# Optimization experiments

Hardware: AMD Instinct MI355X
Metric: run time of the kernel (lower is better)

Reference implementation:

```python
import jax, jax.numpy as jnp
import numpy as np

N_NODES = 100000
N_EDGES = 800000
D_IN, D_HID, D_OUT = 128, 128, 128


def sage_conv(x, edge_index, Wl, bl, Wr):
    # PyG SAGEConv with mean aggregation:
    #   out = lin_l(mean_{j in N(i)} x_j) + lin_r(x_i)
    # x: [N, Din], edge_index: [2, E] (src=row0 -> dst=row1)
    src, dst = edge_index[0], edge_index[1]
    n = x.shape[0]
    msg_sum = jax.ops.segment_sum(x[src], dst, num_segments=n)        # [N, Din]
    deg = jax.ops.segment_sum(jnp.ones((src.shape[0],), x.dtype), dst,
                              num_segments=n)                          # [N]
    agg = msg_sum / jnp.maximum(deg, 1.0)[:, None]
    return agg @ Wl + bl + x @ Wr


def setup_inputs() -> dict:
    key = jax.random.key(0)
    ks = jax.random.split(key, 8)
    s = 1.0 / np.sqrt(D_IN)
    return {
        "x": jax.random.normal(ks[0], (3, N_NODES, D_IN), jnp.float32),
        "edge_index": jax.random.randint(ks[1], (3, 2, N_EDGES), 0, N_NODES,
                                         dtype=jnp.int64),
        "Wl1": jax.random.normal(ks[2], (3, D_IN, D_HID), jnp.float32) * s,
        "bl1": jax.random.normal(ks[3], (3, D_HID), jnp.float32) * s,
        "Wr1": jax.random.normal(ks[4], (3, D_IN, D_HID), jnp.float32) * s,
        "Wl2": jax.random.normal(ks[5], (3, D_HID, D_OUT), jnp.float32) * s,
        "bl2": jax.random.normal(ks[6], (3, D_OUT), jnp.float32) * s,
        "Wr2": jax.random.normal(ks[7], (3, D_HID, D_OUT), jnp.float32) * s,
    }


def reference(x, edge_index, Wl1, bl1, Wr1, Wl2, bl2, Wr2):
    # vmap over the 3 graphs (user-item, social, knowledge)
    conv = jax.vmap(sage_conv)
    h = jax.nn.relu(conv(x, edge_index, Wl1, bl1, Wr1))   # [3, N, hid]
    out = conv(h, edge_index, Wl2, bl2, Wr2)              # [3, N, out]
    # x = ui_x + (s_x + k_x) / 2
    return out[0] + (out[1] + out[2]) / 2
```

## Files before the change

kernel.cpp:

```cpp
#include <hip/hip_runtime.h>

#define N_NODES 100000
#define N_EDGES 800000
#define D 128
#define NBUCK 98
#define CAP 10240
#define QBLK 18750
#define S2B 196
#define QSC 2048.0f
#define IQSC (1.0f / 2048.0f)

typedef __attribute__((ext_vector_type(8))) short short8;
typedef __attribute__((ext_vector_type(4))) float float4_t;
typedef unsigned short ushort_t;

#define MFMA __builtin_amdgcn_mfma_f32_16x16x32_bf16

__device__ __forceinline__ float b2fu(unsigned short u) {
    unsigned int v = ((unsigned int)u) << 16;
    return __builtin_bit_cast(float, v);
}
__device__ __forceinline__ unsigned short f2b(float f) {
    unsigned int u = __builtin_bit_cast(unsigned int, f);
    u = u + 0x7fffu + ((u >> 16) & 1u);
    return (unsigned short)(u >> 16);
}
__device__ __forceinline__ void splitf(float x, unsigned short& h, unsigned short& l) {
    h = f2b(x);
    l = f2b(x - b2fu(h));
}
__device__ __forceinline__ void cvtsplit8(short8 qv, short8& hh, short8& ll) {
#pragma unroll
    for (int j = 0; j < 8; j++) {
        float f = (float)qv[j] * IQSC;
        unsigned short h, l;
        splitf(f, h, l);
        hh[j] = (short)h;
        ll[j] = (short)l;
    }
}

__global__ void setup_kernel(const unsigned int* __restrict__ w, int* __restrict__ flag,
                             int* __restrict__ bucketCount) {
    int t = threadIdx.x;
    if (t == 0) flag[0] = 0;
    for (int i = t; i < 3 * NBUCK; i += 256) bucketCount[i] = 0;
    __syncthreads();
    int any = 0;
    for (int i = t; i < 4096; i += 256)
        if (w[2 * i + 1] != 0) any = 1;
    if (any) atomicOr(flag, 1);
}

__device__ __forceinline__ int ld_idx(const int* w, int f, long j) {
    return f ? w[j] : w[2 * j];
}

__global__ __launch_bounds__(256) void s2q_kernel(const float* __restrict__ X,
                                                  short* __restrict__ XS,
                                                  const int* __restrict__ ei,
                                                  const int* __restrict__ flag,
                                                  int* __restrict__ bucketCount,
                                                  unsigned int* __restrict__ tmp) {
    __shared__ int hist[NBUCK];
    __shared__ int cnt[NBUCK];
    int bxa = blockIdx.x;
    if (bxa < QBLK) {
        size_t i = (size_t)bxa * 256 + threadIdx.x;
        float4 u0 = *(const float4*)(X + i * 8);
        float4 u1 = *(const float4*)(X + i * 8 + 4);
        float vv[8] = {u0.x, u0.y, u0.z, u0.w, u1.x, u1.y, u1.z, u1.w};
        short8 qv;
#pragma unroll
        for (int j = 0; j < 8; j++) {
            int q = __float2int_rn(vv[j] * QSC);
            q = max(-32767, min(32767, q));
            qv[j] = (short)q;
        }
        *(short8*)(XS + i * 8) = qv;
        return;
    }
    int b = bxa - QBLK;
    int g = b / S2B, bx = b % S2B;
    int t = threadIdx.x;
    const int f = flag[0];
    const long j0 = (long)g * 2 * N_EDGES;
    if (t < NBUCK) hist[t] = 0;
    __syncthreads();
#pragma unroll
    for (int it = 0; it < 16; it++) {
        int e = bx * 4096 + it * 256 + t;
        if (e < N_EDGES) {
            int dst = ld_idx(ei, f, j0 + N_EDGES + e);
            atomicAdd(&hist[dst >> 10], 1);
        }
    }
    __syncthreads();
    if (t < NBUCK) cnt[t] = atomicAdd(&bucketCount[g * NBUCK + t], hist[t]);
    __syncthreads();
#pragma unroll
    for (int it = 0; it < 16; it++) {
        int e = bx * 4096 + it * 256 + t;
        if (e < N_EDGES) {
            int src = ld_idx(ei, f, j0 + e);
            int dst = ld_idx(ei, f, j0 + N_EDGES + e);
            int bk = dst >> 10;
            int r = atomicAdd(&cnt[bk], 1);
            if (r < CAP)
                tmp[(size_t)(g * NBUCK + bk) * CAP + r] =
                    (unsigned)src | ((unsigned)(dst & 1023) << 17);
        }
    }
}

__global__ __launch_bounds__(1024) void s3_csr_kernel(const unsigned int* __restrict__ tmp,
                                                      const int* __restrict__ bucketCount,
                                                      int* __restrict__ rowptr,
                                                      int* __restrict__ col) {
    __shared__ int sm[1024];
    __shared__ int pr[1024];
    __shared__ int sbase;
    int b = blockIdx.x, g = blockIdx.y, t = threadIdx.x;
    pr[t] = 0;
    if (t < 128) sm[t] = (t < NBUCK) ? bucketCount[g * NBUCK + t] : 0;
    __syncthreads();
    if (t == 0) {
        int a = 0;
        for (int i = 0; i < b; i++) a += sm[i];
        sbase = a;
    }
    __syncthreads();
    int count = bucketCount[g * NBUCK + b];
    if (count > CAP) count = CAP;
    const unsigned int* recs = tmp + (size_t)(g * NBUCK + b) * CAP;
    for (int i = t; i < count; i += 1024) atomicAdd(&pr[recs[i] >> 17], 1);
    __syncthreads();
    int h = pr[t];
    sm[t] = h;
    __syncthreads();
    for (int off = 1; off < 1024; off <<= 1) {
        int u = (t >= off) ? sm[t - off] : 0;
        __syncthreads();
        sm[t] += u;
        __syncthreads();
    }
    int excl = sm[t] - h;
    int base = sbase;
    int node = b * 1024 + t;
    if (node < N_NODES) rowptr[g * (N_NODES + 1) + node] = base + excl;
    if (b == NBUCK - 1 && t == 0) rowptr[g * (N_NODES + 1) + N_NODES] = N_EDGES;
    __syncthreads();
    pr[t] = base + excl;
    __syncthreads();
    for (int i = t; i < count; i += 1024) {
        unsigned int rec = recs[i];
        int pos = atomicAdd(&pr[rec >> 17], 1);
        col[(size_t)g * N_EDGES + pos] = (int)(rec & 0x1FFFFu);
    }
}

__global__ void packB_kernel(const float* __restrict__ Wl1, const float* __restrict__ Wr1,
                             const float* __restrict__ Wl2, const float* __restrict__ Wr2,
                             ushort_t* __restrict__ Bph, ushort_t* __restrict__ Bpl) {
    int lane = threadIdx.x;
    int tb = blockIdx.x;
    int pidx = blockIdx.y;
    int g = pidx >> 1, layer = pidx & 1;
    const float* Wl = (layer ? Wl2 : Wl1) + (size_t)g * D * D;
    const float* Wr = (layer ? Wr2 : Wr1) + (size_t)g * D * D;
    float scale = (layer && g > 0) ? 0.5f : 1.0f;
    int ks = tb >> 3, nt = tb & 7;
    int n = nt * 16 + (lane & 15);
    int kb = ks * 32 + ((lane >> 4) * 8);
    short8 vh, vl;
#pragma unroll
    for (int j = 0; j < 8; j++) {
        int k = kb + j;
        float wv = ((k < D) ? Wl[k * D + n] : Wr[(k - D) * D + n]) * scale;
        unsigned short h, l;
        splitf(wv, h, l);
        vh[j] = (short)h;
        vl[j] = (short)l;
    }
    size_t o = ((size_t)pidx * 4096 + tb * 64 + lane) * 8;
    *(short8*)(Bph + o) = vh;
    *(short8*)(Bpl + o) = vl;
}

__global__ __launch_bounds__(256) void agg_kernel(const int* __restrict__ rowptr,
                                                  const int* __restrict__ col,
                                                  const short* __restrict__ XS,
                                                  short* __restrict__ AS) {
    int g = blockIdx.y;
    int wid = (int)((blockIdx.x * 256 + threadIdx.x) >> 6);
    if (wid >= N_NODES) return;
    int lane = threadIdx.x & 63;
    int qw = lane >> 4, l4 = lane & 15;
    const int* rp = rowptr + (size_t)g * (N_NODES + 1);
    const int* cle = col + (size_t)g * N_EDGES;
    const short* Xg = XS + (size_t)g * N_NODES * 128;
    int s = rp[wid], e = rp[wid + 1];
    int a0 = 0, a1 = 0, a2 = 0, a3 = 0, a4 = 0, a5 = 0, a6 = 0, a7 = 0;
    for (int i = s + qw; i < e; i += 16) {
        bool p1 = (i + 4) < e, p2 = (i + 8) < e, p3 = (i + 12) < e;
        int c0 = cle[i];
        int c1 = p1 ? cle[i + 4] : c0;
        int c2 = p2 ? cle[i + 8] : c0;
        int c3 = p3 ? cle[i + 12] : c0;
        int4 z = {0, 0, 0, 0};
        int4 v0 = *(const int4*)(Xg + (size_t)c0 * 128 + l4 * 8);
        int4 v1 = p1 ? *(const int4*)(Xg + (size_t)c1 * 128 + l4 * 8) : z;
        int4 v2 = p2 ? *(const int4*)(Xg + (size_t)c2 * 128 + l4 * 8) : z;
        int4 v3 = p3 ? *(const int4*)(Xg + (size_t)c3 * 128 + l4 * 8) : z;
        a0 += (short)v0.x + (short)v1.x + (short)v2.x + (short)v3.x;
        a1 += (v0.x >> 16) + (v1.x >> 16) + (v2.x >> 16) + (v3.x >> 16);
        a2 += (short)v0.y + (short)v1.y + (short)v2.y + (short)v3.y;
        a3 += (v0.y >> 16) + (v1.y >> 16) + (v2.y >> 16) + (v3.y >> 16);
        a4 += (short)v0.z + (short)v1.z + (short)v2.z + (short)v3.z;
        a5 += (v0.z >> 16) + (v1.z >> 16) + (v2.z >> 16) + (v3.z >> 16);
        a6 += (short)v0.w + (short)v1.w + (short)v2.w + (short)v3.w;
        a7 += (v0.w >> 16) + (v1.w >> 16) + (v2.w >> 16) + (v3.w >> 16);
    }
    a0 += __shfl_xor(a0, 16); a1 += __shfl_xor(a1, 16);
    a2 += __shfl_xor(a2, 16); a3 += __shfl_xor(a3, 16);
    a4 += __shfl_xor(a4, 16); a5 += __shfl_xor(a5, 16);
    a6 += __shfl_xor(a6, 16); a7 += __shfl_xor(a7, 16);
    a0 += __shfl_xor(a0, 32); a1 += __shfl_xor(a1, 32);
    a2 += __shfl_xor(a2, 32); a3 += __shfl_xor(a3, 32);
    a4 += __shfl_xor(a4, 32); a5 += __shfl_xor(a5, 32);
    a6 += __shfl_xor(a6, 32); a7 += __shfl_xor(a7, 32);
    if (lane < 16) {
        float invd = (e > s) ? 1.f / (float)(e - s) : 0.f;
        int m0 = __float2int_rn((float)a0 * invd);
        int m1 = __float2int_rn((float)a1 * invd);
        int m2 = __float2int_rn((float)a2 * invd);
        int m3 = __float2int_rn((float)a3 * invd);
        int m4 = __float2int_rn((float)a4 * invd);
        int m5 = __float2int_rn((float)a5 * invd);
        int m6 = __float2int_rn((float)a6 * invd);
        int m7 = __float2int_rn((float)a7 * invd);
        uint4 st;
        st.x = (m0 & 0xffff) | (m1 << 16);
        st.y = (m2 & 0xffff) | (m3 << 16);
        st.z = (m4 & 0xffff) | (m5 << 16);
        st.w = (m6 & 0xffff) | (m7 << 16);
        *(uint4*)(AS + ((size_t)g * N_NODES + wid) * 128 + l4 * 8) = st;
    }
}

__device__ __forceinline__ void gemm_pass(const short* __restrict__ Agg,
                                          const short* __restrict__ Self,
                                          const short8* __restrict__ GH,
                                          const short8* __restrict__ GL,
                                          short8* smH, short8* smL,
                                          int n0, int t, int lane, bool valid,
                                          float4_t acc[2][8]) {
    int r0 = lane & 15, koff = (lane >> 4) * 8;
#pragma unroll
    for (int ks = 0; ks < 8; ks++) {
        __syncthreads();
        smH[t] = GH[ks * 512 + t];
        smH[t + 256] = GH[ks * 512 + t + 256];
        smL[t] = GL[ks * 512 + t];
        smL[t + 256] = GL[ks * 512 + t + 256];
        __syncthreads();
        if (valid) {
            int kk = (ks & 3) * 32 + koff;
            const short* P = (ks < 4) ? Agg : Self;
            short8 q0 = *(const short8*)(P + (size_t)(n0 + r0) * 128 + kk);
            short8 q1 = *(const short8*)(P + (size_t)(n0 + r0 + 16) * 128 + kk);
            short8 a0h, a0l, a1h, a1l;
            cvtsplit8(q0, a0h, a0l);
            cvtsplit8(q1, a1h, a1l);
#pragma unroll
            for (int nt = 0; nt < 8; nt++) {
                short8 wh = smH[nt * 64 + lane];
                short8 wl = smL[nt * 64 + lane];
                acc[0][nt] = MFMA(a0h, wh, acc[0][nt], 0, 0, 0);
                acc[0][nt] = MFMA(a0l, wh, acc[0][nt], 0, 0, 0);
                acc[0][nt] = MFMA(a0h, wl, acc[0][nt], 0, 0, 0);
                acc[1][nt] = MFMA(a1h, wh, acc[1][nt], 0, 0, 0);
                acc[1][nt] = MFMA(a1l, wh, acc[1][nt], 0, 0, 0);
                acc[1][nt] = MFMA(a1h, wl, acc[1][nt], 0, 0, 0);
            }
        }
    }
}

__global__ __launch_bounds__(256) void gemm1_kernel(const short* __restrict__ AS,
                                                    const short* __restrict__ XS,
                                                    const ushort_t* __restrict__ Bph,
                                                    const ushort_t* __restrict__ Bpl,
                                                    const float* __restrict__ bl1,
                                                    short* __restrict__ HS) {
    __shared__ short8 smH[512];
    __shared__ short8 smL[512];
    int g = blockIdx.y;
    int t = threadIdx.x, w = t >> 6, lane = t & 63;
    int n0 = blockIdx.x * 128 + w * 32;
    bool valid = (n0 < N_NODES);

    float4_t acc[2][8];
#pragma unroll
    for (int m = 0; m < 2; m++)
#pragma unroll
        for (int nt = 0; nt < 8; nt++) acc[m][nt] = (float4_t)(0.f);

    gemm_pass(AS + (size_t)g * N_NODES * 128, XS + (size_t)g * N_NODES * 128,
              (const short8*)Bph + (size_t)(g * 2) * 4096,
              (const short8*)Bpl + (size_t)(g * 2) * 4096,
              smH, smL, n0, t, lane, valid, acc);

    if (!valid) return;
    int qq = lane >> 4, c = lane & 15;
    short* Hg = HS + (size_t)g * N_NODES * 128;
#pragma unroll
    for (int m = 0; m < 2; m++)
#pragma unroll
        for (int nt = 0; nt < 8; nt++) {
            int clm = nt * 16 + c;
            float bv = bl1[g * D + clm];
#pragma unroll
            for (int r = 0; r < 4; r++) {
                int row = n0 + m * 16 + qq * 4 + r;
                float v = fmaxf(acc[m][nt][r] + bv, 0.f);
                int qv = __float2int_rn(v * QSC);
                qv = min(qv, 32767);
                Hg[(size_t)row * 128 + clm] = (short)qv;
            }
        }
}

__global__ __launch_bounds__(256) void gemm2_kernel(const short* __restrict__ AS,
                                                    const short* __restrict__ HS,
                                                    const ushort_t* __restrict__ Bph,
                                                    const ushort_t* __restrict__ Bpl,
                                                    const float* __restrict__ bl2,
                                                    float* __restrict__ out) {
    __shared__ short8 smH[512];
    __shared__ short8 smL[512];
    int t = threadIdx.x, w = t >> 6, lane = t & 63;
    int n0 = blockIdx.x * 128 + w * 32;
    bool valid = (n0 < N_NODES);

    float4_t acc[2][8];
#pragma unroll
    for (int m = 0; m < 2; m++)
#pragma unroll
        for (int nt = 0; nt < 8; nt++) acc[m][nt] = (float4_t)(0.f);

#pragma unroll 1
    for (int g = 0; g < 3; g++) {
        gemm_pass(AS + (size_t)g * N_NODES * 128, HS + (size_t)g * N_NODES * 128,
                  (const short8*)Bph + (size_t)(g * 2 + 1) * 4096,
                  (const short8*)Bpl + (size_t)(g * 2 + 1) * 4096,
                  smH, smL, n0, t, lane, valid, acc);
    }

    if (!valid) return;
    int qq = lane >> 4, c = lane & 15;
#pragma unroll
    for (int m = 0; m < 2; m++)
#pragma unroll
        for (int nt = 0; nt < 8; nt++) {
            int clm = nt * 16 + c;
            float bv = bl2[clm] + 0.5f * (bl2[D + clm] + bl2[2 * D + clm]);
#pragma unroll
            for (int r = 0; r < 4; r++) {
                int row = n0 + m * 16 + qq * 4 + r;
                out[(size_t)row * D + clm] = acc[m][nt][r] + bv;
            }
        }
}

extern "C" void kernel_launch(void* const* d_in, const int* in_sizes, int n_in,
                              void* d_out, int out_size, void* d_ws, size_t ws_size,
                              hipStream_t stream) {
    const float* x   = (const float*)d_in[0];
    const int* ei    = (const int*)d_in[1];
    const float* Wl1 = (const float*)d_in[2];
    const float* bl1 = (const float*)d_in[3];
    const float* Wr1 = (const float*)d_in[4];
    const float* Wl2 = (const float*)d_in[5];
    const float* bl2 = (const float*)d_in[6];
    const float* Wr2 = (const float*)d_in[7];
    float* out = (float*)d_out;

    char* p = (char*)d_ws;
    auto alloc = [&](size_t bytes) -> char* {
        char* r = p;
        p += (bytes + 255) & ~(size_t)255;
        return r;
    };
    int* flag        = (int*)alloc(256);
    int* bucketCount = (int*)alloc((size_t)3 * NBUCK * 4);
    int* rowptr      = (int*)alloc((size_t)3 * (N_NODES + 1) * 4);
    int* col         = (int*)alloc((size_t)3 * N_EDGES * 4);
    ushort_t* Bph    = (ushort_t*)alloc((size_t)6 * 32768 * 2);
    ushort_t* Bpl    = (ushort_t*)alloc((size_t)6 * 32768 * 2);
    short* XS        = (short*)alloc((size_t)3 * N_NODES * 128 * 2);
    short* AS        = (short*)alloc((size_t)3 * N_NODES * 128 * 2);
    short* HS        = (short*)alloc((size_t)3 * N_NODES * 128 * 2);
    unsigned int* tmp = (unsigned int*)HS;

    setup_kernel<<<1, 256, 0, stream>>>((const unsigned int*)ei, flag, bucketCount);
    s2q_kernel<<<QBLK + 3 * S2B, 256, 0, stream>>>(x, XS, ei, flag, bucketCount, tmp);
    dim3 s3g(NBUCK, 3);
    s3_csr_kernel<<<s3g, 1024, 0, stream>>>(tmp, bucketCount, rowptr, col);
    packB_kernel<<<dim3(64, 6), 64, 0, stream>>>(Wl1, Wr1, Wl2, Wr2, Bph, Bpl);

    dim3 agrid(N_NODES / 4, 3);
    dim3 ggrid((N_NODES + 127) / 128, 3);
    agg_kernel<<<agrid, 256, 0, stream>>>(rowptr, col, XS, AS);
    gemm1_kernel<<<ggrid, 256, 0, stream>>>(AS, XS, Bph, Bpl, bl1, HS);
    agg_kernel<<<agrid, 256, 0, stream>>>(rowptr, col, HS, AS);
    gemm2_kernel<<<(N_NODES + 127) / 128, 256, 0, stream>>>(AS, HS, Bph, Bpl, bl2, out);
}
```

Baseline: 706.7 us.

## Process two nodes per wave in aggregation, pad zero row, fold weight packing

The aggregation kernel now gives each node half a wavefront instead of a whole one. Each 16-lane group gathers four consecutive neighbours, and missing neighbours point to a new zero padding row instead of using predicated loads. This is meant to reduce idle lanes for low-degree nodes and to remove branches and one shuffle reduction stage. The weight pack/split work moves into extra blocks of the quantisation kernel to save a launch. The X and H buffers grow by one zero row per graph, which shifts their per-graph strides, and index math switches to 32-bit unsigned.

```diff
diff --git a/kernel.cpp b/kernel.cpp
--- a/kernel.cpp
+++ b/kernel.cpp
@@ -7,8 +7,10 @@
 #define CAP 10240
 #define QBLK 18750
 #define S2B 196
+#define PKB 96
 #define QSC 2048.0f
 #define IQSC (1.0f / 2048.0f)
+#define ROWS_G (N_NODES + 1)
 
 typedef __attribute__((ext_vector_type(8))) short short8;
 typedef __attribute__((ext_vector_type(4))) float float4_t;
@@ -41,10 +43,17 @@
 }
 
 __global__ void setup_kernel(const unsigned int* __restrict__ w, int* __restrict__ flag,
-                             int* __restrict__ bucketCount) {
+                             int* __restrict__ bucketCount,
+                             short* __restrict__ XS, short* __restrict__ HS) {
     int t = threadIdx.x;
     if (t == 0) flag[0] = 0;
     for (int i = t; i < 3 * NBUCK; i += 256) bucketCount[i] = 0;
+    for (int i = t; i < 3 * 128; i += 256) {
+        int g = i >> 7, r = i & 127;
+        size_t off = ((size_t)g * ROWS_G + N_NODES) * 128 + r;
+        XS[off] = 0;
+        HS[off] = 0;
+    }
     __syncthreads();
     int any = 0;
     for (int i = t; i < 4096; i += 256)
@@ -61,12 +70,21 @@
                                                   const int* __restrict__ ei,
                                                   const int* __restrict__ flag,
                                                   int* __restrict__ bucketCount,
-                                                  unsigned int* __restrict__ tmp) {
+                                                  unsigned int* __restrict__ tmp,
+                                                  const float* __restrict__ Wl1,
+                                                  const float* __restrict__ Wr1,
+                                                  const float* __restrict__ Wl2,
+                                                  const float* __restrict__ Wr2,
+                                                  ushort_t* __restrict__ Bph,
+                                                  ushort_t* __restrict__ Bpl) {
     __shared__ int hist[NBUCK];
     __shared__ int cnt[NBUCK];
     int bxa = blockIdx.x;
+    int t = threadIdx.x;
     if (bxa < QBLK) {
-        size_t i = (size_t)bxa * 256 + threadIdx.x;
+        size_t i = (size_t)bxa * 256 + t;
+        unsigned g = (unsigned)(i / 1600000u);
+        unsigned loc = (unsigned)i - g * 1600000u;
         float4 u0 = *(const float4*)(X + i * 8);
         float4 u1 = *(const float4*)(X + i * 8 + 4);
         float vv[8] = {u0.x, u0.y, u0.z, u0.w, u1.x, u1.y, u1.z, u1.w};
@@ -77,12 +95,37 @@
             q = max(-32767, min(32767, q));
             qv[j] = (short)q;
         }
-        *(short8*)(XS + i * 8) = qv;
+        *(short8*)(XS + (size_t)g * ROWS_G * 128 + (size_t)loc * 8) = qv;
+        return;
+    }
+    if (bxa >= QBLK + 3 * S2B) {
+        int unit = (bxa - QBLK - 3 * S2B) * 4 + (t >> 6);
+        int lane = t & 63;
+        int tb = unit & 63, pidx = unit >> 6;
+        int g = pidx >> 1, layer = pidx & 1;
+        const float* Wl = (layer ? Wl2 : Wl1) + (size_t)g * D * D;
+        const float* Wr = (layer ? Wr2 : Wr1) + (size_t)g * D * D;
+        float scale = (layer && g > 0) ? 0.5f : 1.0f;
+        int ks = tb >> 3, nt = tb & 7;
+        int n = nt * 16 + (lane & 15);
+        int kb = ks * 32 + ((lane >> 4) * 8);
+        short8 vh, vl;
+#pragma unroll
+        for (int j = 0; j < 8; j++) {
+            int k = kb + j;
+            float wv = ((k < D) ? Wl[k * D + n] : Wr[(k - D) * D + n]) * scale;
+            unsigned short h, l;
+            splitf(wv, h, l);
+            vh[j] = (short)h;
+            vl[j] = (short)l;
+        }
+        size_t o = ((size_t)pidx * 4096 + tb * 64 + lane) * 8;
+        *(short8*)(Bph + o) = vh;
+        *(short8*)(Bpl + o) = vl;
         return;
     }
     int b = bxa - QBLK;
     int g = b / S2B, bx = b % S2B;
-    int t = threadIdx.x;
     const int f = flag[0];
     const long j0 = (long)g * 2 * N_EDGES;
     if (t < NBUCK) hist[t] = 0;
@@ -159,77 +202,43 @@
     }
 }
 
-__global__ void packB_kernel(const float* __restrict__ Wl1, const float* __restrict__ Wr1,
-                             const float* __restrict__ Wl2, const float* __restrict__ Wr2,
-                             ushort_t* __restrict__ Bph, ushort_t* __restrict__ Bpl) {
-    int lane = threadIdx.x;
-    int tb = blockIdx.x;
-    int pidx = blockIdx.y;
-    int g = pidx >> 1, layer = pidx & 1;
-    const float* Wl = (layer ? Wl2 : Wl1) + (size_t)g * D * D;
-    const float* Wr = (layer ? Wr2 : Wr1) + (size_t)g * D * D;
-    float scale = (layer && g > 0) ? 0.5f : 1.0f;
-    int ks = tb >> 3, nt = tb & 7;
-    int n = nt * 16 + (lane & 15);
-    int kb = ks * 32 + ((lane >> 4) * 8);
-    short8 vh, vl;
-#pragma unroll
-    for (int j = 0; j < 8; j++) {
-        int k = kb + j;
-        float wv = ((k < D) ? Wl[k * D + n] : Wr[(k - D) * D + n]) * scale;
-        unsigned short h, l;
-        splitf(wv, h, l);
-        vh[j] = (short)h;
-        vl[j] = (short)l;
-    }
-    size_t o = ((size_t)pidx * 4096 + tb * 64 + lane) * 8;
-    *(short8*)(Bph + o) = vh;
-    *(short8*)(Bpl + o) = vl;
-}
-
 __global__ __launch_bounds__(256) void agg_kernel(const int* __restrict__ rowptr,
                                                   const int* __restrict__ col,
                                                   const short* __restrict__ XS,
                                                   short* __restrict__ AS) {
     int g = blockIdx.y;
-    int wid = (int)((blockIdx.x * 256 + threadIdx.x) >> 6);
-    if (wid >= N_NODES) return;
+    int wv = (int)((blockIdx.x * 256 + threadIdx.x) >> 6);
     int lane = threadIdx.x & 63;
-    int qw = lane >> 4, l4 = lane & 15;
+    int half = lane >> 5, sub = (lane >> 4) & 1, l4 = lane & 15;
+    int node = wv * 2 + half;
     const int* rp = rowptr + (size_t)g * (N_NODES + 1);
     const int* cle = col + (size_t)g * N_EDGES;
-    const short* Xg = XS + (size_t)g * N_NODES * 128;
-    int s = rp[wid], e = rp[wid + 1];
+    const short* Xg = XS + (size_t)g * ROWS_G * 128;
+    int s = rp[node], e = rp[node + 1];
     int a0 = 0, a1 = 0, a2 = 0, a3 = 0, a4 = 0, a5 = 0, a6 = 0, a7 = 0;
-    for (int i = s + qw; i < e; i += 16) {
-        bool p1 = (i + 4) < e, p2 = (i + 8) < e, p3 = (i + 12) < e;
+    for (int i = s + 4 * sub; i < e; i += 8) {
         int c0 = cle[i];
-        int c1 = p1 ? cle[i + 4] : c0;
-        int c2 = p2 ? cle[i + 8] : c0;
-        int c3 = p3 ? cle[i + 12] : c0;
-        int4 z = {0, 0, 0, 0};
-        int4 v0 = *(const int4*)(Xg + (size_t)c0 * 128 + l4 * 8);
-        int4 v1 = p1 ? *(const int4*)(Xg + (size_t)c1 * 128 + l4 * 8) : z;
-        int4 v2 = p2 ? *(const int4*)(Xg + (size_t)c2 * 128 + l4 * 8) : z;
-        int4 v3 = p3 ? *(const int4*)(Xg + (size_t)c3 * 128 + l4 * 8) : z;
-        a0 += (short)v0.x + (short)v1.x + (short)v2.x + (short)v3.x;
-        a1 += (v0.x >> 16) + (v1.x >> 16) + (v2.x >> 16) + (v3.x >> 16);
-        a2 += (short)v0.y + (short)v1.y + (short)v2.y + (short)v3.y;
-        a3 += (v0.y >> 16) + (v1.y >> 16) + (v2.y >> 16) + (v3.y >> 16);
-        a4 += (short)v0.z + (short)v1.z + (short)v2.z + (short)v3.z;
-        a5 += (v0.z >> 16) + (v1.z >> 16) + (v2.z >> 16) + (v3.z >> 16);
-        a6 += (short)v0.w + (short)v1.w + (short)v2.w + (short)v3.w;
-        a7 += (v0.w >> 16) + (v1.w >> 16) + (v2.w >> 16) + (v3.w >> 16);
+        int c1 = (i + 1 < e) ? cle[i + 1] : N_NODES;
+        int c2 = (i + 2 < e) ? cle[i + 2] : N_NODES;
+        int c3 = (i + 3 < e) ? cle[i + 3] : N_NODES;
+        int4 v0 = *(const int4*)(Xg + (unsigned)c0 * 128u + l4 * 8);
+        int4 v1 = *(const int4*)(Xg + (unsigned)c1 * 128u + l4 * 8);
+        int4 v2 = *(const int4*)(Xg + (unsigned)c2 * 128u + l4 * 8);
+        int4 v3 = *(const int4*)(Xg + (unsigned)c3 * 128u + l4 * 8);
+        a0 += ((short)v0.x + (short)v1.x) + ((short)v2.x + (short)v3.x);
+        a1 += ((v0.x >> 16) + (v1.x >> 16)) + ((v2.x >> 16) + (v3.x >> 16));
+        a2 += ((short)v0.y + (short)v1.y) + ((short)v2.y + (short)v3.y);
+        a3 += ((v0.y >> 16) + (v1.y >> 16)) + ((v2.y >> 16) + (v3.y >> 16));
+        a4 += ((short)v0.z + (short)v1.z) + ((short)v2.z + (short)v3.z);
+        a5 += ((v0.z >> 16) + (v1.z >> 16)) + ((v2.z >> 16) + (v3.z >> 16));
+        a6 += ((short)v0.w + (short)v1.w) + ((short)v2.w + (short)v3.w);
+        a7 += ((v0.w >> 16) + (v1.w >> 16)) + ((v2.w >> 16) + (v3.w >> 16));
     }
     a0 += __shfl_xor(a0, 16); a1 += __shfl_xor(a1, 16);
     a2 += __shfl_xor(a2, 16); a3 += __shfl_xor(a3, 16);
     a4 += __shfl_xor(a4, 16); a5 += __shfl_xor(a5, 16);
     a6 += __shfl_xor(a6, 16); a7 += __shfl_xor(a7, 16);
-    a0 += __shfl_xor(a0, 32); a1 += __shfl_xor(a1, 32);
-    a2 += __shfl_xor(a2, 32); a3 += __shfl_xor(a3, 32);
-    a4 += __shfl_xor(a4, 32); a5 += __shfl_xor(a5, 32);
-    a6 += __shfl_xor(a6, 32); a7 += __shfl_xor(a7, 32);
-    if (lane < 16) {
+    if (sub == 0) {
         float invd = (e > s) ? 1.f / (float)(e - s) : 0.f;
         int m0 = __float2int_rn((float)a0 * invd);
         int m1 = __float2int_rn((float)a1 * invd);
@@ -244,7 +253,7 @@
         st.y = (m2 & 0xffff) | (m3 << 16);
         st.z = (m4 & 0xffff) | (m5 << 16);
         st.w = (m6 & 0xffff) | (m7 << 16);
-        *(uint4*)(AS + ((size_t)g * N_NODES + wid) * 128 + l4 * 8) = st;
+        *(uint4*)(AS + ((size_t)g * N_NODES + node) * 128 + l4 * 8) = st;
     }
 }
 
@@ -267,8 +276,8 @@
         if (valid) {
             int kk = (ks & 3) * 32 + koff;
             const short* P = (ks < 4) ? Agg : Self;
-            short8 q0 = *(const short8*)(P + (size_t)(n0 + r0) * 128 + kk);
-            short8 q1 = *(const short8*)(P + (size_t)(n0 + r0 + 16) * 128 + kk);
+            short8 q0 = *(const short8*)(P + (unsigned)(n0 + r0) * 128u + kk);
+            short8 q1 = *(const short8*)(P + (unsigned)(n0 + r0 + 16) * 128u + kk);
             short8 a0h, a0l, a1h, a1l;
             cvtsplit8(q0, a0h, a0l);
             cvtsplit8(q1, a1h, a1l);
@@ -306,14 +315,14 @@
 #pragma unroll
         for (int nt = 0; nt < 8; nt++) acc[m][nt] = (float4_t)(0.f);
 
-    gemm_pass(AS + (size_t)g * N_NODES * 128, XS + (size_t)g * N_NODES * 128,
+    gemm_pass(AS + (size_t)g * N_NODES * 128, XS + (size_t)g * ROWS_G * 128,
               (const short8*)Bph + (size_t)(g * 2) * 4096,
               (const short8*)Bpl + (size_t)(g * 2) * 4096,
               smH, smL, n0, t, lane, valid, acc);
 
     if (!valid) return;
     int qq = lane >> 4, c = lane & 15;
-    short* Hg = HS + (size_t)g * N_NODES * 128;
+    short* Hg = HS + (size_t)g * ROWS_G * 128;
 #pragma unroll
     for (int m = 0; m < 2; m++)
 #pragma unroll
@@ -351,7 +360,7 @@
 
 #pragma unroll 1
     for (int g = 0; g < 3; g++) {
-        gemm_pass(AS + (size_t)g * N_NODES * 128, HS + (size_t)g * N_NODES * 128,
+        gemm_pass(AS + (size_t)g * N_NODES * 128, HS + (size_t)g * ROWS_G * 128,
                   (const short8*)Bph + (size_t)(g * 2 + 1) * 4096,
                   (const short8*)Bpl + (size_t)(g * 2 + 1) * 4096,
                   smH, smL, n0, t, lane, valid, acc);
@@ -395,21 +404,23 @@
     int* flag        = (int*)alloc(256);
     int* bucketCount = (int*)alloc((size_t)3 * NBUCK * 4);
     int* rowptr      = (int*)alloc((size_t)3 * (N_NODES + 1) * 4);
-    int* col         = (int*)alloc((size_t)3 * N_EDGES * 4);
+    int* col         = (int*)alloc((size_t)3 * N_EDGES * 4 + 16);
     ushort_t* Bph    = (ushort_t*)alloc((size_t)6 * 32768 * 2);
     ushort_t* Bpl    = (ushort_t*)alloc((size_t)6 * 32768 * 2);
-    short* XS        = (short*)alloc((size_t)3 * N_NODES * 128 * 2);
+    short* XS        = (short*)alloc((size_t)3 * ROWS_G * 128 * 2);
     short* AS        = (short*)alloc((size_t)3 * N_NODES * 128 * 2);
-    short* HS        = (short*)alloc((size_t)3 * N_NODES * 128 * 2);
+    short* HS        = (short*)alloc((size_t)3 * ROWS_G * 128 * 2);
     unsigned int* tmp = (unsigned int*)HS;
 
-    setup_kernel<<<1, 256, 0, stream>>>((const unsigned int*)ei, flag, bucketCount);
-    s2q_kernel<<<QBLK + 3 * S2B, 256, 0, stream>>>(x, XS, ei, flag, bucketCount, tmp);
+    setup_kernel<<<1, 256, 0, stream>>>((const unsigned int*)ei, flag, bucketCount,
+                                        XS, HS);
+    s2q_kernel<<<QBLK + 3 * S2B + PKB, 256, 0, stream>>>(x, XS, ei, flag, bucketCount,
+                                                         tmp, Wl1, Wr1, Wl2, Wr2,
+                                                         Bph, Bpl);
     dim3 s3g(NBUCK, 3);
     s3_csr_kernel<<<s3g, 1024, 0, stream>>>(tmp, bucketCount, rowptr, col);
-    packB_kernel<<<dim3(64, 6), 64, 0, stream>>>(Wl1, Wr1, Wl2, Wr2, Bph, Bpl);
-
-    dim3 agrid(N_NODES / 4, 3);
+
+    dim3 agrid(N_NODES / 8, 3);
     dim3 ggrid((N_NODES + 127) / 128, 3);
     agg_kernel<<<agrid, 256, 0, stream>>>(rowptr, col, XS, AS);
     gemm1_kernel<<<ggrid, 256, 0, stream>>>(AS, XS, Bph, Bpl, bl1, HS);
```

New measurement: 649.3 us. -8.1%, faster.
